# Kernel tuning notes

Hardware: AMD Instinct MI355X
Metric: run time of the kernel (lower is better)

The kernel has to match this reference:

```python
import jax, jax.numpy as jnp
import numpy as np

N = 20000
NEG_SLOPE = 0.2


def gatv2_layer(x, src, dst, edge_attr, Wl, bl, Wr, br, We, att, bias, H, C):
    """PyG GATv2Conv: add self-loops (edge_attr fill='mean'), gather-score-softmax-aggregate."""
    n = x.shape[0]
    E = src.shape[0]
    # --- add self loops, self-loop edge_attr = mean of incoming edge_attr per node ---
    ea_sum = jax.ops.segment_sum(edge_attr, dst, num_segments=n)
    deg = jax.ops.segment_sum(jnp.ones((E, 1), x.dtype), dst, num_segments=n)
    ea_loop = ea_sum / jnp.maximum(deg, 1.0)
    loop = jnp.arange(n)
    src_a = jnp.concatenate([src, loop])
    dst_a = jnp.concatenate([dst, loop])
    ea = jnp.concatenate([edge_attr, ea_loop], axis=0)
    # --- linear projections ---
    xl = (x @ Wl + bl).reshape(n, H, C)   # source-side features
    xr = (x @ Wr + br).reshape(n, H, C)   # target-side features
    e = (ea @ We).reshape(-1, H, C)       # edge features
    # --- per-edge GATv2 attention score ---
    m = xl[src_a] + xr[dst_a] + e                          # [E', H, C]
    s = jnp.sum(jax.nn.leaky_relu(m, NEG_SLOPE) * att, -1)  # [E', H]
    # --- softmax over incoming edges of each target node ---
    smax = jax.ops.segment_max(s, dst_a, num_segments=n)
    ex = jnp.exp(s - smax[dst_a])
    denom = jax.ops.segment_sum(ex, dst_a, num_segments=n)
    alpha = ex / (denom[dst_a] + 1e-16)                    # [E', H]
    # --- aggregate messages (alpha * x_l[src]) ---
    out = jax.ops.segment_sum(alpha[..., None] * xl[src_a], dst_a, num_segments=n)
    return out.reshape(n, H * C) + bias


def setup_inputs() -> dict:
    key = jax.random.key(0)
    ks = jax.random.split(key, 20)
    F, HID, H1, A = 128, 32, 8, 128
    E = 640000
    d = {}
    d["x"] = jax.random.normal(ks[0], (N, F), jnp.float32)
    d["edge_index"] = jax.random.randint(ks[1], (2, E), 0, N, jnp.int32).astype(jnp.int64)
    d["edge_attr"] = jax.random.normal(ks[2], (E, 1), jnp.float32)
    # layer 1 params (in=F, out=HID, heads=H1)
    d["W1l"] = jax.random.normal(ks[3], (F, H1 * HID), jnp.float32) * 0.05
    d["b1l"] = jnp.zeros((H1 * HID,), jnp.float32)
    d["W1r"] = jax.random.normal(ks[4], (F, H1 * HID), jnp.float32) * 0.05
    d["b1r"] = jnp.zeros((H1 * HID,), jnp.float32)
    d["We1"] = jax.random.normal(ks[5], (1, H1 * HID), jnp.float32) * 0.05
    d["att1"] = jax.random.normal(ks[6], (H1, HID), jnp.float32) * 0.05
    d["bias1"] = jnp.zeros((H1 * HID,), jnp.float32)
    # layer 2 params (in=H1*HID, out=A, heads=1)
    d["W2l"] = jax.random.normal(ks[7], (H1 * HID, A), jnp.float32) * 0.05
    d["b2l"] = jnp.zeros((A,), jnp.float32)
    d["W2r"] = jax.random.normal(ks[8], (H1 * HID, A), jnp.float32) * 0.05
    d["b2r"] = jnp.zeros((A,), jnp.float32)
    d["We2"] = jax.random.normal(ks[9], (1, A), jnp.float32) * 0.05
    d["att2"] = jax.random.normal(ks[10], (1, A), jnp.float32) * 0.05
    d["bias2"] = jnp.zeros((A,), jnp.float32)
    d["alpha"] = jnp.array(0.0, jnp.float32)
    return d


def reference(x, edge_index, edge_attr, W1l, b1l, W1r, b1r, We1, att1, bias1,
              W2l, b2l, W2r, b2r, We2, att2, bias2, alpha):
    src, dst = edge_index[0], edge_index[1]
    h = jax.nn.relu(gatv2_layer(x, src, dst, edge_attr, W1l, b1l, W1r, b1r,
                                We1, att1, bias1, H=8, C=32))
    h = jax.nn.relu(gatv2_layer(h, src, dst, edge_attr, W2l, b2l, W2r, b2r,
                                We2, att2, bias2, H=1, C=128))
    pooled = jnp.mean(h, axis=0, keepdims=True)  # global_mean_pool, single graph -> [1, A]
    return jax.nn.softmax(pooled, axis=1), jax.nn.sigmoid(alpha)
```

## Files before the change

kernel.cpp:

```cpp
#include <hip/hip_runtime.h>
#include <math.h>

#define NEG_SLOPE 0.2f

typedef __attribute__((ext_vector_type(8))) short short8;
typedef __attribute__((ext_vector_type(4))) float f32x4;

__device__ __forceinline__ int imin(int a, int b) { return a < b ? a : b; }

__device__ __forceinline__ unsigned int f2bf(float f) {
    unsigned int u = __float_as_uint(f);
    return (u + 0x7fffu + ((u >> 16) & 1u)) >> 16;
}
__device__ __forceinline__ void bf2f(unsigned int u, float& a, float& b) {
    a = __uint_as_float(u << 16);
    b = __uint_as_float(u & 0xffff0000u);
}
template <int CTRL>
__device__ __forceinline__ float dpp_add(float v) {
    int t = __builtin_amdgcn_update_dpp(0, __float_as_int(v), CTRL, 0xF, 0xF, true);
    return v + __int_as_float(t);
}

__global__ void edge_hist(const int* __restrict__ ei, const float* __restrict__ ea,
                          unsigned long long* __restrict__ hist, int E) {
    int e = blockIdx.x * blockDim.x + threadIdx.x;
    if (e < E) {
        int d = ei[E + e];
        long long fx = (long long)__float2int_rn(ea[e] * 65536.0f);
        unsigned long long v = ((unsigned long long)fx << 32) | 1ull;
        atomicAdd(&hist[(size_t)d * 8], v);
    }
}

__global__ void scan_a(const unsigned long long* __restrict__ hist, int* __restrict__ bsum, int n) {
    __shared__ int wred[4];
    int base = blockIdx.x * 1024;
    int tid = threadIdx.x;
    int s = 0;
#pragma unroll
    for (int k = 0; k < 4; ++k) {
        int i = base + tid + k * 256;
        if (i < n) s += (int)(hist[(size_t)i * 8] & 0xffffffffull);
    }
#pragma unroll
    for (int off = 32; off > 0; off >>= 1) s += __shfl_xor(s, off, 64);
    if ((tid & 63) == 0) wred[tid >> 6] = s;
    __syncthreads();
    if (tid == 0) bsum[blockIdx.x] = wred[0] + wred[1] + wred[2] + wred[3];
}

__global__ void scan_b(int* __restrict__ bsum, int* __restrict__ row_ptr, int B, int n) {
    int tid = threadIdx.x;
    int v = (tid < B) ? bsum[tid] : 0;
    int s = v;
#pragma unroll
    for (int off = 1; off < 64; off <<= 1) {
        int t = __shfl_up(s, off, 64);
        if (tid >= off) s += t;
    }
    if (tid < B) bsum[tid] = s - v;
    if (tid == 63) row_ptr[n] = s;
}

__global__ void scan_c(const unsigned long long* __restrict__ hist,
                       const int* __restrict__ bsum, int* __restrict__ row_ptr,
                       int* __restrict__ wptr_pad, float* __restrict__ ea_loop, int n) {
    __shared__ int wtot[4];
    int tid = threadIdx.x;
    int wid = tid >> 6, lane = tid & 63;
    int i0 = blockIdx.x * 1024 + tid * 4;
    int dcnt[4]; float esum[4];
#pragma unroll
    for (int k = 0; k < 4; ++k) {
        if (i0 + k < n) {
            unsigned long long h = hist[(size_t)(i0 + k) * 8];
            dcnt[k] = (int)(h & 0xffffffffull);
            esum[k] = (float)((int)(h >> 32)) * (1.0f / 65536.0f);
        } else { dcnt[k] = 0; esum[k] = 0.0f; }
    }
    int tsum = dcnt[0] + dcnt[1] + dcnt[2] + dcnt[3];
    int s = tsum;
#pragma unroll
    for (int off = 1; off < 64; off <<= 1) {
        int t = __shfl_up(s, off, 64);
        if (lane >= off) s += t;
    }
    if (lane == 63) wtot[wid] = s;
    __syncthreads();
    int wpre = 0;
#pragma unroll
    for (int k = 0; k < 4; ++k) if (k < wid) wpre += wtot[k];
    int pre = bsum[blockIdx.x] + wpre + (s - tsum);
    if (i0 < n) {
        int4 e;
        e.x = pre;
        e.y = pre + dcnt[0];
        e.z = e.y + dcnt[1];
        e.w = e.z + dcnt[2];
        *(int4*)(row_ptr + i0) = e;
        int ev[4] = { e.x, e.y, e.z, e.w };
        float4 el;
        el.x = esum[0] / fmaxf((float)dcnt[0], 1.0f);
        el.y = esum[1] / fmaxf((float)dcnt[1], 1.0f);
        el.z = esum[2] / fmaxf((float)dcnt[2], 1.0f);
        el.w = esum[3] / fmaxf((float)dcnt[3], 1.0f);
        *(float4*)(ea_loop + i0) = el;
#pragma unroll
        for (int k = 0; k < 4; ++k) wptr_pad[(size_t)(i0 + k) * 16] = ev[k];
    }
}

__global__ void edge_scatter(const int* __restrict__ ei, const float* __restrict__ ea,
                             int* __restrict__ wptr_pad, int2* __restrict__ spk, int E) {
    int e = blockIdx.x * blockDim.x + threadIdx.x;
    if (e < E) {
        int d = ei[E + e];
        int pos = atomicAdd(&wptr_pad[(size_t)d * 16], 1);
        spk[pos] = make_int2(ei[e], __float_as_int(ea[e]));
    }
}

__global__ void cvt_bf16_v4(const float* __restrict__ in, unsigned short* __restrict__ out, int sz4) {
    int i = blockIdx.x * blockDim.x + threadIdx.x;
    if (i < sz4) {
        float4 v = ((const float4*)in)[i];
        uint2 r;
        r.x = f2bf(v.x) | (f2bf(v.y) << 16);
        r.y = f2bf(v.z) | (f2bf(v.w) << 16);
        ((uint2*)out)[i] = r;
    }
}
__global__ void tr_cvt_bf16(const float* __restrict__ in, unsigned short* __restrict__ out,
                            int K, int N) {
    int i = blockIdx.x * blockDim.x + threadIdx.x;
    if (i < K * N) {
        int k = i / N, nn = i - k * N;
        out[nn * K + k] = (unsigned short)f2bf(in[i]);
    }
}
__global__ void bias_cat(const float* __restrict__ a, const float* __restrict__ b,
                         float* __restrict__ out, int na, int ntot) {
    int i = blockIdx.x * blockDim.x + threadIdx.x;
    if (i < ntot) out[i] = (i < na) ? a[i] : b[i - na];
}

__global__ void __launch_bounds__(256)
gemm_bf16(const unsigned short* __restrict__ A, const unsigned short* __restrict__ Bt,
          const float* __restrict__ bias, unsigned short* __restrict__ C,
          int M, int N, int K) {
    __shared__ __attribute__((aligned(16))) unsigned short As[64 * 40];
    __shared__ __attribute__((aligned(16))) unsigned short Bs[64 * 40];
    int tid  = threadIdx.x;
    int wave = tid >> 6, lane = tid & 63;
    int m0 = blockIdx.x * 64, n0 = blockIdx.y * 64;
    int row = tid >> 2, kg = (tid & 3) * 8;

    f32x4 acc[4] = {};
    for (int kk = 0; kk < K; kk += 32) {
        int gm = m0 + row;
        uint4 av;
        if (gm < M) av = *(const uint4*)(A + (size_t)gm * K + kk + kg);
        else        av = make_uint4(0, 0, 0, 0);
        *(uint4*)&As[row * 40 + kg] = av;
        uint4 bv = *(const uint4*)(Bt + (size_t)(n0 + row) * K + kk + kg);
        *(uint4*)&Bs[row * 40 + kg] = bv;
        __syncthreads();
        short8 a = *(const short8*)&As[(wave * 16 + (lane & 15)) * 40 + (lane >> 4) * 8];
#pragma unroll
        for (int g = 0; g < 4; ++g) {
            short8 b = *(const short8*)&Bs[(g * 16 + (lane & 15)) * 40 + (lane >> 4) * 8];
            acc[g] = __builtin_amdgcn_mfma_f32_16x16x32_bf16(a, b, acc[g], 0, 0, 0);
        }
        __syncthreads();
    }
#pragma unroll
    for (int g = 0; g < 4; ++g) {
        int col = n0 + g * 16 + (lane & 15);
        float bs = bias[col];
#pragma unroll
        for (int r = 0; r < 4; ++r) {
            int grow = m0 + wave * 16 + (lane >> 4) * 4 + r;
            if (grow < M) C[(size_t)grow * N + col] = (unsigned short)f2bf(acc[g][r] + bs);
        }
    }
}

template <int NV>
__device__ __forceinline__ void ld_row(float* r, const float* p) {
    if constexpr (NV == 4) {
        float4 t = *(const float4*)p;
        r[0] = t.x; r[1] = t.y; r[2] = t.z; r[3] = t.w;
    } else {
        float2 t = *(const float2*)p;
        r[0] = t.x; r[1] = t.y;
    }
}
template <int NV>
__device__ __forceinline__ uint2 ld_bf(const unsigned short* __restrict__ base, int laneoff) {
    uint2 r;
    if constexpr (NV == 4) r = *(const uint2*)(base + laneoff);
    else { r.x = *(const unsigned int*)(base + laneoff); r.y = 0; }
    return r;
}
template <int G>
__device__ __forceinline__ float grp_reduce(float vs) {
    vs = dpp_add<0xB1>(vs);
    vs = dpp_add<0x4E>(vs);
    vs = dpp_add<0x141>(vs);
    if constexpr (G >= 16) vs = dpp_add<0x140>(vs);
    if constexpr (G >= 32) {
        int t = __builtin_amdgcn_ds_swizzle(__float_as_int(vs), 0x401F);
        vs += __int_as_float(t);
    }
    if constexpr (G >= 64) vs += __shfl_xor(vs, 32, 64);
    return vs;
}

template <int HC, int STRIDE, int C, bool OUT_BF16>
__global__ void __launch_bounds__(256)
gat_agg(const unsigned short* __restrict__ xlr,
        const float* __restrict__ We, const float* __restrict__ att,
        const float* __restrict__ bias,
        const int* __restrict__ row_ptr, const int2* __restrict__ spk,
        const float* __restrict__ ea_loop,
        void* __restrict__ out, int n) {
    constexpr int NV = HC / 64;
    constexpr int G  = C / NV;
    int wave = threadIdx.x >> 6;
    int lane = threadIdx.x & 63;
    int node = blockIdx.x * 4 + wave;
    if (node >= n) return;
    int laneoff = lane * NV;

    float xr_r[NV], We_r[NV], att6[NV], att4[NV], o[NV];
    {
        uint2 u = ld_bf<NV>(xlr + (size_t)node * STRIDE + HC, laneoff);
        if constexpr (NV == 4) { bf2f(u.x, xr_r[0], xr_r[1]); bf2f(u.y, xr_r[2], xr_r[3]); }
        else                   { bf2f(u.x, xr_r[0], xr_r[1]); }
    }
    ld_row<NV>(We_r, We + laneoff);
    {
        float att_r[NV];
        ld_row<NV>(att_r, att + laneoff);
#pragma unroll
        for (int j = 0; j < NV; ++j) { att6[j] = 0.6f * att_r[j]; att4[j] = 0.4f * att_r[j]; }
    }

    int start = __builtin_amdgcn_readfirstlane(row_ptr[node]);
    int end   = __builtin_amdgcn_readfirstlane(row_ptr[node + 1]);
    float ea_l = ea_loop[node];
    float l = 0.0f;
#pragma unroll
    for (int j = 0; j < NV; ++j) o[j] = 0.0f;

    auto process = [&](uint2 xu, float w) {
        float xf[NV];
        if constexpr (NV == 4) { bf2f(xu.x, xf[0], xf[1]); bf2f(xu.y, xf[2], xf[3]); }
        else                   { bf2f(xu.x, xf[0], xf[1]); }
        float vs = 0.0f;
#pragma unroll
        for (int j = 0; j < NV; ++j) {
            float mm = xf[j] + fmaf(w, We_r[j], xr_r[j]);
            vs = fmaf(att6[j], mm, vs);
            vs = fmaf(att4[j], fabsf(mm), vs);
        }
        vs = grp_reduce<G>(vs);
        float pr = __expf(vs);
        l += pr;
#pragma unroll
        for (int j = 0; j < NV; ++j) o[j] = fmaf(pr, xf[j], o[j]);
    };

    process(ld_bf<NV>(xlr + (size_t)node * STRIDE, laneoff), ea_l);

    int cnt = end - start;
    for (int b0 = 0; b0 < cnt; b0 += 64) {
        int rem = imin(64, cnt - b0);
        int idx = start + b0 + lane;
        int idxc = imin(idx, end - 1);
        int2 pv = spk[idxc];

        auto rl = [&](int j) {
            int s = __builtin_amdgcn_readlane(pv.x, j);
            return ld_bf<NV>(xlr + (size_t)s * STRIDE, laneoff);
        };
        auto rw = [&](int j) {
            return __int_as_float(__builtin_amdgcn_readlane(pv.y, j));
        };

        int rc = rem - 1;
        uint2 X0 = rl(0),            X1 = rl(imin(1, rc)),
              X2 = rl(imin(2, rc)),  X3 = rl(imin(3, rc));
        float W0 = rw(0),            W1 = rw(imin(1, rc)),
              W2 = rw(imin(2, rc)),  W3 = rw(imin(3, rc));

        int j = 0;
        for (; j + 4 <= rem; j += 4) {
            uint2 Y0 = rl(imin(j + 4, rc)), Y1 = rl(imin(j + 5, rc)),
                  Y2 = rl(imin(j + 6, rc)), Y3 = rl(imin(j + 7, rc));
            float U0 = rw(imin(j + 4, rc)), U1 = rw(imin(j + 5, rc)),
                  U2 = rw(imin(j + 6, rc)), U3 = rw(imin(j + 7, rc));
            process(X0, W0); process(X1, W1); process(X2, W2); process(X3, W3);
            X0 = Y0; X1 = Y1; X2 = Y2; X3 = Y3;
            W0 = U0; W1 = U1; W2 = U2; W3 = U3;
        }
        if (j < rem) {
            process(X0, W0);
            if (j + 1 < rem) {
                process(X1, W1);
                if (j + 2 < rem) process(X2, W2);
            }
        }
    }

    float inv = 1.0f / (l + 1e-16f);
    float b_r[NV];
    ld_row<NV>(b_r, bias + laneoff);
    float v[NV];
#pragma unroll
    for (int j = 0; j < NV; ++j) v[j] = fmaxf(o[j] * inv + b_r[j], 0.0f);

    if constexpr (OUT_BF16) {
        unsigned short* op = (unsigned short*)out + (size_t)node * HC + laneoff;
        if constexpr (NV == 4) {
            uint2 t;
            t.x = f2bf(v[0]) | (f2bf(v[1]) << 16);
            t.y = f2bf(v[2]) | (f2bf(v[3]) << 16);
            *(uint2*)op = t;
        } else {
            *(unsigned int*)op = f2bf(v[0]) | (f2bf(v[1]) << 16);
        }
    } else {
        float* op = (float*)out + (size_t)node * HC + laneoff;
        if constexpr (NV == 4) { *(float4*)op = make_float4(v[0], v[1], v[2], v[3]); }
        else                   { *(float2*)op = make_float2(v[0], v[1]); }
    }
}

__global__ void pool_partial(const float* __restrict__ h2, float* __restrict__ partial, int n) {
    int t = threadIdx.x;
    float s = 0.0f;
    for (int r = blockIdx.x; r < n; r += gridDim.x) s += h2[(size_t)r * 128 + t];
    partial[blockIdx.x * 128 + t] = s;
}

__global__ void __launch_bounds__(1024)
pool_final(const float* __restrict__ partial, int nb,
           const float* __restrict__ alpha_in,
           float* __restrict__ out, int n) {
    __shared__ float acc[8][128];
    __shared__ float red[4];
    int t = threadIdx.x & 127;
    int g = threadIdx.x >> 7;
    float s = 0.0f;
    for (int b = g; b < nb; b += 8) s += partial[b * 128 + t];
    acc[g][t] = s;
    __syncthreads();
    if (threadIdx.x < 128) {
        float tot = 0.0f;
#pragma unroll
        for (int k = 0; k < 8; ++k) tot += acc[k][t];
        float mean = tot / (float)n;
        float mx = mean;
#pragma unroll
        for (int off = 32; off > 0; off >>= 1) mx = fmaxf(mx, __shfl_xor(mx, off, 64));
        if ((t & 63) == 0) red[t >> 6] = mx;
        __syncthreads();
        mx = fmaxf(red[0], red[1]);
        float ex = __expf(mean - mx);
        float sm = ex;
#pragma unroll
        for (int off = 32; off > 0; off >>= 1) sm += __shfl_xor(sm, off, 64);
        if ((t & 63) == 0) red[2 + (t >> 6)] = sm;
        __syncthreads();
        sm = red[2] + red[3];
        out[t] = ex / sm;
        if (t == 0) out[128] = 1.0f / (1.0f + __expf(-alpha_in[0]));
    }
}

extern "C" void kernel_launch(void* const* d_in, const int* in_sizes, int n_in,
                              void* d_out, int out_size, void* d_ws, size_t ws_size,
                              hipStream_t stream) {
    const float* x    = (const float*)d_in[0];
    const int*   ei   = (const int*)d_in[1];
    const float* ea   = (const float*)d_in[2];
    const float* W1l  = (const float*)d_in[3];
    const float* b1l  = (const float*)d_in[4];
    const float* W1r  = (const float*)d_in[5];
    const float* b1r  = (const float*)d_in[6];
    const float* We1  = (const float*)d_in[7];
    const float* att1 = (const float*)d_in[8];
    const float* bias1= (const float*)d_in[9];
    const float* W2l  = (const float*)d_in[10];
    const float* b2l  = (const float*)d_in[11];
    const float* W2r  = (const float*)d_in[12];
    const float* b2r  = (const float*)d_in[13];
    const float* We2  = (const float*)d_in[14];
    const float* att2 = (const float*)d_in[15];
    const float* bias2= (const float*)d_in[16];
    const float* alpha= (const float*)d_in[17];
    float* out = (float*)d_out;

    const int F = 128, HC1 = 256, HC2 = 128;
    const int n = in_sizes[0] / F;
    const int E = in_sizes[1] / 2;
    const int B = (n + 1023) / 1024;

    char* ws = (char*)d_ws;
    size_t off = 0;
    auto alloc = [&](size_t bytes) { size_t p = off; off += (bytes + 255) & ~(size_t)255; return p; };

    unsigned long long* hist = (unsigned long long*)(ws + alloc((size_t)n * 8 * 8));
    int*   row_ptr = (int*)  (ws + alloc((size_t)(n + 1) * 4));
    int*   wptr    = (int*)  (ws + alloc((size_t)n * 16 * 4));
    float* ea_loop = (float*)(ws + alloc((size_t)n * 4));
    int*   bsum    = (int*)  (ws + alloc(64 * 4));
    int2*  spk     = (int2*) (ws + alloc((size_t)E * 8));
    unsigned short* xb   = (unsigned short*)(ws + alloc((size_t)n * F * 2));
    unsigned short* Wt1  = (unsigned short*)(ws + alloc((size_t)F * (2 * HC1) * 2));
    unsigned short* Wt2  = (unsigned short*)(ws + alloc((size_t)HC1 * (2 * HC2) * 2));
    float* b1cat   = (float*)(ws + alloc((size_t)2 * HC1 * 4));
    float* b2cat   = (float*)(ws + alloc((size_t)2 * HC2 * 4));
    unsigned short* xlr1 = (unsigned short*)(ws + alloc((size_t)n * 2 * HC1 * 2));
    unsigned short* h1   = (unsigned short*)(ws + alloc((size_t)n * HC1 * 2));
    float* h2      = (float*)(ws + alloc((size_t)n * HC2 * 4));
    float* partial = (float*)(ws + alloc((size_t)256 * 128 * 4));
    unsigned short* xlr2 = xlr1;
    const int NB_POOL = 256;

    (void)hipMemsetAsync(hist, 0, (size_t)n * 8 * 8, stream);

    int tb = 256;
    edge_hist<<<(E + tb - 1) / tb, tb, 0, stream>>>(ei, ea, hist, E);
    scan_a<<<B, 256, 0, stream>>>(hist, bsum, n);
    scan_b<<<1, 64, 0, stream>>>(bsum, row_ptr, B, n);
    scan_c<<<B, 256, 0, stream>>>(hist, bsum, row_ptr, wptr, ea_loop, n);
    edge_scatter<<<(E + tb - 1) / tb, tb, 0, stream>>>(ei, ea, wptr, spk, E);

    cvt_bf16_v4<<<(n * F / 4 + tb - 1) / tb, tb, 0, stream>>>(x, xb, n * F / 4);
    tr_cvt_bf16<<<(F * HC1 + tb - 1) / tb, tb, 0, stream>>>(W1l, Wt1, F, HC1);
    tr_cvt_bf16<<<(F * HC1 + tb - 1) / tb, tb, 0, stream>>>(W1r, Wt1 + (size_t)HC1 * F, F, HC1);
    tr_cvt_bf16<<<(HC1 * HC2 + tb - 1) / tb, tb, 0, stream>>>(W2l, Wt2, HC1, HC2);
    tr_cvt_bf16<<<(HC1 * HC2 + tb - 1) / tb, tb, 0, stream>>>(W2r, Wt2 + (size_t)HC2 * HC1, HC1, HC2);
    bias_cat<<<(2 * HC1 + tb - 1) / tb, tb, 0, stream>>>(b1l, b1r, b1cat, HC1, 2 * HC1);
    bias_cat<<<(2 * HC2 + tb - 1) / tb, tb, 0, stream>>>(b2l, b2r, b2cat, HC2, 2 * HC2);

    {
        dim3 grid((n + 63) / 64, (2 * HC1) / 64);
        gemm_bf16<<<grid, 256, 0, stream>>>(xb, Wt1, b1cat, xlr1, n, 2 * HC1, F);
    }
    gat_agg<256, 512, 32, true><<<(n + 3) / 4, 256, 0, stream>>>(
        xlr1, We1, att1, bias1, row_ptr, spk, ea_loop, h1, n);

    {
        dim3 grid((n + 63) / 64, (2 * HC2) / 64);
        gemm_bf16<<<grid, 256, 0, stream>>>(h1, Wt2, b2cat, xlr2, n, 2 * HC2, HC1);
    }
    gat_agg<128, 256, 128, false><<<(n + 3) / 4, 256, 0, stream>>>(
        xlr2, We2, att2, bias2, row_ptr, spk, ea_loop, h2, n);

    pool_partial<<<NB_POOL, 128, 0, stream>>>(h2, partial, n);
    pool_final<<<1, 1024, 0, stream>>>(partial, NB_POOL, alpha, out, n);
}
```

Measured before the change: 319.3 us.

## Deepen edge gather prefetch to 8, use exp2 with prescaled attention, fuse weight prep

The neighbor gather loop in gat_agg now prefetches 8 source rows ahead instead of 4, so more loads are in flight and latency is better hidden. The attention weights are pre-multiplied by log2(e) so the per-edge exponential becomes a plain exp2. The six small weight-transpose and bias-concat launches are merged into a single prep_weights kernel to cut launch overhead. The deeper prefetch uses more registers, which may lower occupancy, and a fixed 8-wide tail is processed for short neighbor lists.

Measured after the change: 321.9 us. About the same (+0.8%).

```diff
diff --git a/kernel.cpp b/kernel.cpp
--- a/kernel.cpp
+++ b/kernel.cpp
@@ -2,6 +2,7 @@
 #include <math.h>
 
 #define NEG_SLOPE 0.2f
+#define LOG2E 1.4426950408889634f
 
 typedef __attribute__((ext_vector_type(8))) short short8;
 typedef __attribute__((ext_vector_type(4))) float f32x4;
@@ -131,18 +132,38 @@
         ((uint2*)out)[i] = r;
     }
 }
-__global__ void tr_cvt_bf16(const float* __restrict__ in, unsigned short* __restrict__ out,
-                            int K, int N) {
+
+__global__ void prep_weights(const float* __restrict__ W1l, const float* __restrict__ W1r,
+                             const float* __restrict__ W2l, const float* __restrict__ W2r,
+                             const float* __restrict__ b1l, const float* __restrict__ b1r,
+                             const float* __restrict__ b2l, const float* __restrict__ b2r,
+                             unsigned short* __restrict__ Wt1, unsigned short* __restrict__ Wt2,
+                             float* __restrict__ b1cat, float* __restrict__ b2cat,
+                             int F, int HC1, int HC2) {
+    int S1 = F * HC1, S2 = HC1 * HC2;
     int i = blockIdx.x * blockDim.x + threadIdx.x;
-    if (i < K * N) {
-        int k = i / N, nn = i - k * N;
-        out[nn * K + k] = (unsigned short)f2bf(in[i]);
-    }
-}
-__global__ void bias_cat(const float* __restrict__ a, const float* __restrict__ b,
-                         float* __restrict__ out, int na, int ntot) {
-    int i = blockIdx.x * blockDim.x + threadIdx.x;
-    if (i < ntot) out[i] = (i < na) ? a[i] : b[i - na];
+    if (i < S1) {
+        int k = i / HC1, nn = i - k * HC1;
+        Wt1[(size_t)nn * F + k] = (unsigned short)f2bf(W1l[i]);
+    } else if (i < 2 * S1) {
+        int j = i - S1;
+        int k = j / HC1, nn = j - k * HC1;
+        Wt1[(size_t)(HC1 + nn) * F + k] = (unsigned short)f2bf(W1r[j]);
+    } else if (i < 2 * S1 + S2) {
+        int j = i - 2 * S1;
+        int k = j / HC2, nn = j - k * HC2;
+        Wt2[(size_t)nn * HC1 + k] = (unsigned short)f2bf(W2l[j]);
+    } else if (i < 2 * S1 + 2 * S2) {
+        int j = i - 2 * S1 - S2;
+        int k = j / HC2, nn = j - k * HC2;
+        Wt2[(size_t)(HC2 + nn) * HC1 + k] = (unsigned short)f2bf(W2r[j]);
+    } else if (i < 2 * S1 + 2 * S2 + 2 * HC1) {
+        int j = i - 2 * S1 - 2 * S2;
+        b1cat[j] = (j < HC1) ? b1l[j] : b1r[j - HC1];
+    } else if (i < 2 * S1 + 2 * S2 + 2 * HC1 + 2 * HC2) {
+        int j = i - 2 * S1 - 2 * S2 - 2 * HC1;
+        b2cat[j] = (j < HC2) ? b2l[j] : b2r[j - HC2];
+    }
 }
 
 __global__ void __launch_bounds__(256)
@@ -236,28 +257,31 @@
     float xr_r[NV], We_r[NV], att6[NV], att4[NV], o[NV];
     {
         uint2 u = ld_bf<NV>(xlr + (size_t)node * STRIDE + HC, laneoff);
-        if constexpr (NV == 4) { bf2f(u.x, xr_r[0], xr_r[1]); bf2f(u.y, xr_r[2], xr_r[3]); }
-        else                   { bf2f(u.x, xr_r[0], xr_r[1]); }
+        bf2f(u.x, xr_r[0], xr_r[1]);
+        if constexpr (NV == 4) bf2f(u.y, xr_r[2], xr_r[3]);
     }
     ld_row<NV>(We_r, We + laneoff);
     {
         float att_r[NV];
         ld_row<NV>(att_r, att + laneoff);
 #pragma unroll
-        for (int j = 0; j < NV; ++j) { att6[j] = 0.6f * att_r[j]; att4[j] = 0.4f * att_r[j]; }
-    }
+        for (int j = 0; j < NV; ++j) {
+            att6[j] = 0.6f * LOG2E * att_r[j];
+            att4[j] = 0.4f * LOG2E * att_r[j];
+        }
+    }
+#pragma unroll
+    for (int j = 0; j < NV; ++j) o[j] = 0.0f;
 
     int start = __builtin_amdgcn_readfirstlane(row_ptr[node]);
     int end   = __builtin_amdgcn_readfirstlane(row_ptr[node + 1]);
     float ea_l = ea_loop[node];
     float l = 0.0f;
-#pragma unroll
-    for (int j = 0; j < NV; ++j) o[j] = 0.0f;
 
     auto process = [&](uint2 xu, float w) {
         float xf[NV];
-        if constexpr (NV == 4) { bf2f(xu.x, xf[0], xf[1]); bf2f(xu.y, xf[2], xf[3]); }
-        else                   { bf2f(xu.x, xf[0], xf[1]); }
+        bf2f(xu.x, xf[0], xf[1]);
+        if constexpr (NV == 4) bf2f(xu.y, xf[2], xf[3]);
         float vs = 0.0f;
 #pragma unroll
         for (int j = 0; j < NV; ++j) {
@@ -266,7 +290,7 @@
             vs = fmaf(att4[j], fabsf(mm), vs);
         }
         vs = grp_reduce<G>(vs);
-        float pr = __expf(vs);
+        float pr = exp2f(vs);
         l += pr;
 #pragma unroll
         for (int j = 0; j < NV; ++j) o[j] = fmaf(pr, xf[j], o[j]);
@@ -290,27 +314,29 @@
         };
 
         int rc = rem - 1;
-        uint2 X0 = rl(0),            X1 = rl(imin(1, rc)),
-              X2 = rl(imin(2, rc)),  X3 = rl(imin(3, rc));
-        float W0 = rw(0),            W1 = rw(imin(1, rc)),
-              W2 = rw(imin(2, rc)),  W3 = rw(imin(3, rc));
+        uint2 X[8]; float Wv[8];
+#pragma unroll
+        for (int k = 0; k < 8; ++k) {
+            int t = imin(k, rc);
+            X[k] = rl(t); Wv[k] = rw(t);
+        }
 
         int j = 0;
-        for (; j + 4 <= rem; j += 4) {
-            uint2 Y0 = rl(imin(j + 4, rc)), Y1 = rl(imin(j + 5, rc)),
-                  Y2 = rl(imin(j + 6, rc)), Y3 = rl(imin(j + 7, rc));
-            float U0 = rw(imin(j + 4, rc)), U1 = rw(imin(j + 5, rc)),
-                  U2 = rw(imin(j + 6, rc)), U3 = rw(imin(j + 7, rc));
-            process(X0, W0); process(X1, W1); process(X2, W2); process(X3, W3);
-            X0 = Y0; X1 = Y1; X2 = Y2; X3 = Y3;
-            W0 = U0; W1 = U1; W2 = U2; W3 = U3;
-        }
-        if (j < rem) {
-            process(X0, W0);
-            if (j + 1 < rem) {
-                process(X1, W1);
-                if (j + 2 < rem) process(X2, W2);
+        for (; j + 8 <= rem; j += 8) {
+            uint2 Y[8]; float U[8];
+#pragma unroll
+            for (int k = 0; k < 8; ++k) {
+                int t = imin(j + 8 + k, rc);
+                Y[k] = rl(t); U[k] = rw(t);
             }
+#pragma unroll
+            for (int k = 0; k < 8; ++k) process(X[k], Wv[k]);
+#pragma unroll
+            for (int k = 0; k < 8; ++k) { X[k] = Y[k]; Wv[k] = U[k]; }
+        }
+#pragma unroll
+        for (int k = 0; k < 8; ++k) {
+            if (j + k < rem) process(X[k], Wv[k]);
         }
     }
 
@@ -440,12 +466,11 @@
     edge_scatter<<<(E + tb - 1) / tb, tb, 0, stream>>>(ei, ea, wptr, spk, E);
 
     cvt_bf16_v4<<<(n * F / 4 + tb - 1) / tb, tb, 0, stream>>>(x, xb, n * F / 4);
-    tr_cvt_bf16<<<(F * HC1 + tb - 1) / tb, tb, 0, stream>>>(W1l, Wt1, F, HC1);
-    tr_cvt_bf16<<<(F * HC1 + tb - 1) / tb, tb, 0, stream>>>(W1r, Wt1 + (size_t)HC1 * F, F, HC1);
-    tr_cvt_bf16<<<(HC1 * HC2 + tb - 1) / tb, tb, 0, stream>>>(W2l, Wt2, HC1, HC2);
-    tr_cvt_bf16<<<(HC1 * HC2 + tb - 1) / tb, tb, 0, stream>>>(W2r, Wt2 + (size_t)HC2 * HC1, HC1, HC2);
-    bias_cat<<<(2 * HC1 + tb - 1) / tb, tb, 0, stream>>>(b1l, b1r, b1cat, HC1, 2 * HC1);
-    bias_cat<<<(2 * HC2 + tb - 1) / tb, tb, 0, stream>>>(b2l, b2r, b2cat, HC2, 2 * HC2);
+    {
+        int total = 2 * F * HC1 + 2 * HC1 * HC2 + 2 * HC1 + 2 * HC2;
+        prep_weights<<<(total + tb - 1) / tb, tb, 0, stream>>>(
+            W1l, W1r, W2l, W2r, b1l, b1r, b2l, b2r, Wt1, Wt2, b1cat, b2cat, F, HC1, HC2);
+    }
 
     {
         dim3 grid((n + 63) / 64, (2 * HC1) / 64);
```
